# Kernel optimization log

Measured on AMD Instinct MI355X. Metric: run time of the kernel, lower is better.

Reference implementation:

```python
import jax, jax.numpy as jnp
import numpy as np

MODEL_DIM = 1024
HIDDEN = 2048
NUM_GROUPS = 2
EXPERTS_PER_GP = 4
NUM_EXPERTS = NUM_GROUPS * EXPERTS_PER_GP
TOP_K = 2
B, T = 2, 2048


def _swiglu(x):
    a, b = jnp.split(x, 2, axis=-1)
    return jax.nn.silu(a) * b


def setup_inputs() -> dict:
    key = jax.random.key(0)
    ks = jax.random.split(key, 7)
    s = 0.02  # init scale
    return {
        "x": jax.random.normal(ks[0], (B, T, MODEL_DIM), jnp.float32),
        # torch Linear weight layout [out_features, in_features]
        "w_in": jax.random.normal(ks[1], (HIDDEN * 2, MODEL_DIM), jnp.float32) * s,   # shared_in
        "w_out": jax.random.normal(ks[2], (MODEL_DIM, HIDDEN), jnp.float32) * s,      # shared_out
        "w1": jax.random.normal(ks[3], (HIDDEN * 2, MODEL_DIM), jnp.float32) * s,     # w1_shared
        "w2": jax.random.normal(ks[4], (NUM_EXPERTS, MODEL_DIM, HIDDEN), jnp.float32) * s,  # w2_expert stack
        "wg": jax.random.normal(ks[5], (NUM_GROUPS, MODEL_DIM), jnp.float32) * s,     # group_gate
        "we": jax.random.normal(ks[6], (NUM_EXPERTS, MODEL_DIM), jnp.float32) * s,    # expert_gate
        "gb": jnp.zeros((NUM_GROUPS,), jnp.float32),   # group_bias
        "eb": jnp.zeros((NUM_EXPERTS,), jnp.float32),  # expert_bias
    }


def reference(x, w_in, w_out, w1, w2, wg, we, gb, eb):
    Bs, Ts, C = x.shape
    S = Bs * Ts
    flat = x.reshape(S, C)

    # shared expert path
    shared = _swiglu(flat @ w_in.T) @ w_out.T                    # [S, C]

    # level-1: group gate (top-1)
    g_probs = jax.nn.softmax(flat @ wg.T + gb, axis=-1)          # [S, G]
    g_idx = jnp.argmax(g_probs, axis=-1)                         # [S]

    # level-2: expert gate masked to the chosen group
    e_logits = flat @ we.T + eb                                  # [S, E]
    egid = jnp.arange(NUM_EXPERTS) // EXPERTS_PER_GP             # expert -> group id
    masked = jnp.where(g_idx[:, None] == egid[None, :], e_logits, -jnp.inf)
    e_probs = jax.nn.softmax(masked, axis=-1)                    # zero outside group

    g_prob = jnp.take_along_axis(g_probs, g_idx[:, None], axis=1)  # [S, 1]
    p_expert = e_probs * g_prob                                  # [S, E]

    topv, topi = jax.lax.top_k(p_expert, TOP_K)                  # [S, k]

    # per-token per-expert combine weight (dense [S, E], rows k-sparse)
    w_se = jnp.zeros((S, NUM_EXPERTS), x.dtype).at[
        jnp.arange(S)[:, None], topi].add(topv)

    # w1 is shared across experts -> compute hidden once for all tokens
    h = _swiglu(flat @ w1.T)                                     # [S, H]

    # routed = sum_e w_se[:, e] * (h @ w2[e].T); scale commutes through linear
    routed = jnp.zeros_like(shared)
    for e in range(NUM_EXPERTS):  # small fixed expert count
        routed = routed + (h * w_se[:, e:e + 1]) @ w2[e].T

    return (shared + routed).reshape(Bs, Ts, C)
```

## Files before the change

kernel.cpp:

```cpp
#include <hip/hip_runtime.h>
#include <math.h>


#define C_DIM 1024
#define H_DIM 2048
#define S_TOK 4096

typedef _Float16 f16x8 __attribute__((ext_vector_type(8)));
typedef float f32x4 __attribute__((ext_vector_type(4)));

#define AS3(p) ((__attribute__((address_space(3))) void*)(p))
#define AS1c(p) ((const __attribute__((address_space(1))) void*)(p))

__global__ __launch_bounds__(256) void cvt_all(
    const float* __restrict__ x, const float* __restrict__ w_in,
    const float* __restrict__ w1, const float* __restrict__ w_out,
    const float* __restrict__ w2, _Float16* __restrict__ xh,
    _Float16* __restrict__ wprime, _Float16* __restrict__ wouth,
    _Float16* __restrict__ w2h) {
  int i = blockIdx.x * 256 + threadIdx.x;
  const float* s; _Float16* d; size_t soff, doff;
  if (i < 524288) { s = x; d = xh; soff = doff = (size_t)i; }
  else if (i < 1572864) {
    int n = i - 524288;
    int out_row = n >> 7, kc = n & 127;
    int wmat = out_row >> 12, r = out_row & 4095;
    int g = r >> 5, ii = r & 31;
    int src_row = (ii < 16) ? (g * 16 + ii) : (2048 + g * 16 + (ii - 16));
    s = wmat ? w1 : w_in; d = wprime;
    soff = (size_t)src_row * 128 + kc;
    doff = (size_t)n;
  } else if (i < 1835008) { int n = i - 1572864; s = w_out; d = wouth; soff = doff = (size_t)n; }
  else { int n = i - 1835008; s = w2; d = w2h; soff = doff = (size_t)n; }
  const float4* sp = reinterpret_cast<const float4*>(s) + soff * 2;
  float4 a = sp[0], b = sp[1];
  f16x8 h;
  h[0] = (_Float16)a.x; h[1] = (_Float16)a.y; h[2] = (_Float16)a.z; h[3] = (_Float16)a.w;
  h[4] = (_Float16)b.x; h[5] = (_Float16)b.y; h[6] = (_Float16)b.z; h[7] = (_Float16)b.w;
  reinterpret_cast<f16x8*>(d)[doff] = h;
}

__global__ __launch_bounds__(256) void gate_kernel(const float* __restrict__ x,
    const float* __restrict__ wg, const float* __restrict__ we,
    const float* __restrict__ gb, const float* __restrict__ eb,
    int* __restrict__ top2_e, float* __restrict__ top2_w) {
  const int lane = threadIdx.x & 63;
  const int token = blockIdx.x * 4 + (threadIdx.x >> 6);
  const float* xr = x + (size_t)token * C_DIM + lane * 16;
  float xv[16];
#pragma unroll
  for (int i = 0; i < 16; i += 4) {
    float4 t = *reinterpret_cast<const float4*>(xr + i);
    xv[i] = t.x; xv[i + 1] = t.y; xv[i + 2] = t.z; xv[i + 3] = t.w;
  }
  float dots[10];
#pragma unroll
  for (int g = 0; g < 10; ++g) {
    const float* wr = (g < 2 ? wg + (size_t)g * C_DIM : we + (size_t)(g - 2) * C_DIM) + lane * 16;
    float d = 0.f;
#pragma unroll
    for (int i = 0; i < 16; i += 4) {
      float4 t = *reinterpret_cast<const float4*>(wr + i);
      d += xv[i] * t.x + xv[i + 1] * t.y + xv[i + 2] * t.z + xv[i + 3] * t.w;
    }
#pragma unroll
    for (int off = 32; off > 0; off >>= 1) d += __shfl_xor(d, off);
    dots[g] = d;
  }
  if (lane != 0) return;
  float g0 = dots[0] + gb[0], g1 = dots[1] + gb[1];
  int gidx = (g0 >= g1) ? 0 : 1;
  float gm = fmaxf(g0, g1);
  float ex0 = expf(g0 - gm), ex1 = expf(g1 - gm);
  float gprob = (gidx == 0 ? ex0 : ex1) / (ex0 + ex1);
  const int base = gidx * 4;
  float el[4];
  float m = -1e30f;
#pragma unroll
  for (int jj = 0; jj < 4; ++jj) { el[jj] = dots[2 + base + jj] + eb[base + jj]; m = fmaxf(m, el[jj]); }
  float s = 0.f;
#pragma unroll
  for (int jj = 0; jj < 4; ++jj) { el[jj] = expf(el[jj] - m); s += el[jj]; }
  float p[8];
#pragma unroll
  for (int e = 0; e < 8; ++e) p[e] = 0.f;
#pragma unroll
  for (int jj = 0; jj < 4; ++jj) p[base + jj] = el[jj] / s * gprob;
  int i1 = 0; float v1 = -1.f;
#pragma unroll
  for (int e = 0; e < 8; ++e) if (p[e] > v1) { v1 = p[e]; i1 = e; }
  int i2 = -1; float v2 = -1.f;
#pragma unroll
  for (int e = 0; e < 8; ++e) if (e != i1 && p[e] > v2) { v2 = p[e]; i2 = e; }
  top2_e[token * 2] = i1;     top2_w[token * 2] = v1;
  top2_e[token * 2 + 1] = i2; top2_w[token * 2 + 1] = v2;
}

__global__ __launch_bounds__(256) void scanfill(const int* __restrict__ top2_e,
    const float* __restrict__ top2_w, int* __restrict__ offs_g,
    int* __restrict__ tok_list, float* __restrict__ scale_list,
    int* __restrict__ tok2slot) {
  __shared__ int cnt[8], offs[9], cur[8];
  const int tid = threadIdx.x;
  if (tid < 8) { cnt[tid] = 0; cur[tid] = 0; }
  __syncthreads();
  for (int i = tid; i < 2 * S_TOK; i += 256) atomicAdd(&cnt[top2_e[i]], 1);
  __syncthreads();
  if (tid == 0) {
    offs[0] = 0;
    for (int e = 0; e < 8; ++e) offs[e + 1] = offs[e] + cnt[e];
    for (int e = 0; e < 9; ++e) offs_g[e] = offs[e];
  }
  __syncthreads();
  for (int i = tid; i < 2 * S_TOK; i += 256) {
    int e = top2_e[i];
    int slot = atomicAdd(&cur[e], 1);
    int g = offs[e] + slot;
    tok_list[g] = i >> 1;
    scale_list[g] = top2_w[i];
    tok2slot[i] = g;
  }
}

__device__ __forceinline__ f16x8 frag_ld(const _Float16* t, int row, int u) {
  return *reinterpret_cast<const f16x8*>(t + row * 64 + ((u ^ (row & 7)) << 3));
}

#define BAR __builtin_amdgcn_s_barrier()
#define LGKM0 do { asm volatile("s_waitcnt lgkmcnt(0)" ::: "memory"); \
                   __builtin_amdgcn_sched_barrier(0); } while (0)
#define PRI1 __builtin_amdgcn_s_setprio(1)
#define PRI0 __builtin_amdgcn_s_setprio(0)

#define STAGEA(h_, t_) do { \
  const _Float16* s_ = aS[h_] + (size_t)(t_) * 64; \
  _Float16* d_ = lds + ((t_) & 1) * 32768 + (h_) * 8192 + grp0; \
  __builtin_amdgcn_global_load_lds(AS1c(s_), AS3(d_), 16, 0, 0); \
  __builtin_amdgcn_global_load_lds(AS1c(s_ + 65536), AS3(d_ + 4096), 16, 0, 0); \
} while (0)
#define STAGEB(h_, t_) do { \
  const _Float16* s_ = bS[h_] + (size_t)(t_) * 64; \
  _Float16* d_ = lds + ((t_) & 1) * 32768 + 16384 + (h_) * 8192 + grp0; \
  __builtin_amdgcn_global_load_lds(AS1c(s_), AS3(d_), 16, 0, 0); \
  __builtin_amdgcn_global_load_lds(AS1c(s_ + 65536), AS3(d_ + 4096), 16, 0, 0); \
} while (0)

#define LDA(MB_) do { _Pragma("unroll") for (int mm = 0; mm < 4; ++mm) \
  { _Pragma("unroll") for (int ks = 0; ks < 2; ++ks) \
    af[mm][ks] = frag_ld(At, wm * 128 + (MB_) + mm * 16 + lr, ks * 4 + lq); } } while (0)
#define LDB(DST_, CB_) do { _Pragma("unroll") for (int nn = 0; nn < 2; ++nn) \
  { _Pragma("unroll") for (int ks = 0; ks < 2; ++ks) \
    DST_[nn][ks] = frag_ld(Bt, wn * 64 + (CB_) + nn * 16 + lr, ks * 4 + lq); } } while (0)
#define QUAD(MB_, BF_, NB_) do { \
  _Pragma("unroll") for (int ks = 0; ks < 2; ++ks) \
  _Pragma("unroll") for (int mm = 0; mm < 4; ++mm) \
  _Pragma("unroll") for (int nn = 0; nn < 2; ++nn) \
    acc[(MB_) + mm][(NB_) + nn] = __builtin_amdgcn_mfma_f32_16x16x32_f16( \
        af[mm][ks], BF_[nn][ks], acc[(MB_) + mm][(NB_) + nn], 0, 0, 0); \
} while (0)

__global__ __launch_bounds__(512, 2) void gemm_fused_swiglu(
    const _Float16* __restrict__ A, const _Float16* __restrict__ Wp,
    _Float16* __restrict__ H1, _Float16* __restrict__ H2) {
  __shared__ _Float16 lds[65536];
  const int tid = threadIdx.x;
  const int lane = tid & 63;
  const int wid = tid >> 6;
  const int wm = wid >> 2, wn = wid & 3;
  const int lr = lane & 15, lq = lane >> 4;

  const int bid = blockIdx.x;
  const int xcd = bid & 7, j = bid >> 3;
  const int nb = xcd * 4 + (j & 3);
  const int mb = j >> 2;
  const int row0 = mb * 256;
  const int colg0 = nb * 256;

  const int rA = tid >> 3, uA = tid & 7;
  const int grp0 = (tid & ~63) << 3;
  const int swz = (uA ^ (rA & 7)) << 3;
  const _Float16* aS[2];
  const _Float16* bS[2];
#pragma unroll
  for (int h = 0; h < 2; ++h) {
    aS[h] = A  + (size_t)(row0  + h * 128 + rA) * 1024 + swz;
    bS[h] = Wp + (size_t)(colg0 + h * 128 + rA) * 1024 + swz;
  }

  STAGEB(0, 0); STAGEB(1, 0); STAGEA(0, 0); STAGEA(1, 0);
  STAGEB(0, 1); STAGEB(1, 1); STAGEA(0, 1); STAGEA(1, 1);
  asm volatile("s_waitcnt vmcnt(8)" ::: "memory");
  BAR;

  f32x4 acc[8][4] = {};
  f16x8 af[4][2], bf[2][2], bf2[2][2];

  for (int t = 0; t < 16; ++t) {
    const _Float16* At = lds + (t & 1) * 32768;
    const _Float16* Bt = At + 16384;
    LDA(0); LDB(bf, 0);
    BAR; LGKM0; PRI1; QUAD(0, bf, 0); PRI0; BAR;
    LDB(bf2, 32);
    BAR; LGKM0; PRI1; QUAD(0, bf2, 2); PRI0; BAR;
    LDA(64);
    if (t < 14) { STAGEB(0, t + 2); STAGEB(1, t + 2); }
    BAR; LGKM0; PRI1; QUAD(4, bf, 0); PRI0; BAR;
    if (t < 14) { STAGEA(0, t + 2); STAGEA(1, t + 2); }
    BAR; PRI1; QUAD(4, bf2, 2); PRI0;
    if (t <= 13) { asm volatile("s_waitcnt vmcnt(8)" ::: "memory"); }
    else if (t == 14) { asm volatile("s_waitcnt vmcnt(0)" ::: "memory"); }
    BAR;
  }

  _Float16* Hd = (colg0 >= 4096) ? H2 : H1;
  const int col0h = (colg0 & 4095) >> 1;
#pragma unroll
  for (int mm = 0; mm < 8; ++mm)
#pragma unroll
    for (int np = 0; np < 2; ++np)
#pragma unroll
      for (int r = 0; r < 4; ++r) {
        float a = acc[mm][np * 2][r];
        float b = acc[mm][np * 2 + 1][r];
        float h = (a / (1.0f + __expf(-a))) * b;
        int row = wm * 128 + mm * 16 + lq * 4 + r;
        int hcol = wn * 32 + np * 16 + lr;
        lds[row * 128 + ((((hcol >> 3) ^ (row & 7)) << 3) | (hcol & 7))] = (_Float16)h;
      }
  __syncthreads();
#pragma unroll
  for (int i = 0; i < 8; ++i) {
    int c = tid + i * 512;
    int row = c >> 4, bblk = c & 15;
    f16x8 v = *reinterpret_cast<const f16x8*>(lds + row * 128 + ((bblk ^ (row & 7)) << 3));
    *reinterpret_cast<f16x8*>(Hd + (size_t)(row0 + row) * H_DIM + col0h + bblk * 8) = v;
  }
}

#define OSTAGE(t_) do { int buf_ = ((t_) & 1) * 8192; \
  _Pragma("unroll") for (int i_ = 0; i_ < 2; ++i_) { \
    __builtin_amdgcn_global_load_lds(AS1c(aG[i_] + (size_t)(t_) * 64), AS3(aL[i_] + buf_), 16, 0, 0); \
    __builtin_amdgcn_global_load_lds(AS1c(bG[i_] + (size_t)(t_) * 64), AS3(bL[i_] + buf_), 16, 0, 0); } \
} while (0)

__global__ __launch_bounds__(512, 4) void gemm_out(
    const _Float16* __restrict__ H1, const _Float16* __restrict__ H2,
    const _Float16* __restrict__ Wout, const _Float16* __restrict__ W2,
    const int* __restrict__ offs_g, const int* __restrict__ tok_list,
    const float* __restrict__ scale_list,
    float* __restrict__ out, _Float16* __restrict__ routed) {
  __shared__ _Float16 AtF[2 * 128 * 64];
  __shared__ _Float16 BtF[2 * 128 * 64];
  __shared__ float sse[128];
  const int tid = threadIdx.x;
  const int lane = tid & 63;
  const int wid = tid >> 6;
  const int wm = wid >> 2, wn = wid & 3;
  const int lr = lane & 15, lq = lane >> 4;

  const int b = blockIdx.x;
  const bool shared_role = (b < 256);
  int rb, cb, offs_e = 0, n_e = 0;
  const _Float16* Bp;
  if (shared_role) {
    rb = b >> 3; cb = b & 7;
    Bp = Wout;
  } else {
    int eb2 = b - 256;
    int e = eb2 >> 8; rb = (eb2 >> 3) & 31; cb = eb2 & 7;
    offs_e = offs_g[e]; n_e = offs_g[e + 1] - offs_e;
    if (rb * 128 >= n_e) return;
    Bp = W2 + (size_t)e * C_DIM * H_DIM;
    if (tid < 128) {
      int lrr = rb * 128 + tid;
      sse[tid] = (lrr < n_e) ? scale_list[offs_e + lrr] : 0.f;
    }
  }

  const _Float16* aG[2];
  const _Float16* bG[2];
  _Float16* aL[2];
  _Float16* bL[2];
#pragma unroll
  for (int i = 0; i < 2; ++i) {
    int c = tid + i * 512;
    int row = c >> 3, u = c & 7;
    int swz = (u ^ (row & 7)) << 3;
    const _Float16* rowbase;
    if (shared_role) {
      rowbase = H1 + (size_t)(rb * 128 + row) * H_DIM;
    } else {
      int lrr = rb * 128 + row;
      int gs = offs_e + (lrr < n_e ? lrr : n_e - 1);
      rowbase = H2 + (size_t)tok_list[gs] * H_DIM;
    }
    aG[i] = rowbase + swz;
    bG[i] = Bp + (size_t)(cb * 128 + row) * H_DIM + swz;
    aL[i] = AtF + ((c & ~63) << 3);
    bL[i] = BtF + ((c & ~63) << 3);
  }

  OSTAGE(0); OSTAGE(1);
  asm volatile("s_waitcnt vmcnt(4)" ::: "memory");
  BAR;

  f32x4 acc[4][2] = {};
  for (int t = 0; t < 32; ++t) {
    const _Float16* Ab = AtF + (t & 1) * 8192;
    const _Float16* Bb = BtF + (t & 1) * 8192;
    f16x8 af[4][2], bfr[2][2];
#pragma unroll
    for (int m = 0; m < 4; ++m)
#pragma unroll
      for (int ks = 0; ks < 2; ++ks)
        af[m][ks] = frag_ld(Ab, wm * 64 + m * 16 + lr, ks * 4 + lq);
#pragma unroll
    for (int n = 0; n < 2; ++n)
#pragma unroll
      for (int ks = 0; ks < 2; ++ks)
        bfr[n][ks] = frag_ld(Bb, wn * 32 + n * 16 + lr, ks * 4 + lq);
    BAR; LGKM0;
    PRI1;
#pragma unroll
    for (int m = 0; m < 4; ++m)
#pragma unroll
      for (int n = 0; n < 2; ++n)
        acc[m][n] = __builtin_amdgcn_mfma_f32_16x16x32_f16(af[m][0], bfr[n][0], acc[m][n], 0, 0, 0);
    PRI0;
    BAR;
    if (t < 30) OSTAGE(t + 2);
    BAR;
    PRI1;
#pragma unroll
    for (int m = 0; m < 4; ++m)
#pragma unroll
      for (int n = 0; n < 2; ++n)
        acc[m][n] = __builtin_amdgcn_mfma_f32_16x16x32_f16(af[m][1], bfr[n][1], acc[m][n], 0, 0, 0);
    PRI0;
    if (t < 30) { asm volatile("s_waitcnt vmcnt(4)" ::: "memory"); }
    else if (t == 30) { asm volatile("s_waitcnt vmcnt(0)" ::: "memory"); }
    BAR;
  }

#pragma unroll
  for (int m = 0; m < 4; ++m)
#pragma unroll
    for (int n = 0; n < 2; ++n)
#pragma unroll
      for (int r = 0; r < 4; ++r) {
        int rloc = wm * 64 + m * 16 + (lq << 2) + r;
        int col = cb * 128 + wn * 32 + n * 16 + lr;
        if (shared_role) {
          out[(size_t)(rb * 128 + rloc) * C_DIM + col] = acc[m][n][r];
        } else {
          int lrr = rb * 128 + rloc;
          if (lrr < n_e)
            routed[(size_t)(offs_e + lrr) * C_DIM + col] =
                (_Float16)(sse[rloc] * acc[m][n][r]);
        }
      }
}

__global__ __launch_bounds__(256) void combine_final(float* __restrict__ out,
    const _Float16* __restrict__ routed, const int* __restrict__ tok2slot) {
  const int t = blockIdx.x * 2 + (threadIdx.x >> 7);
  const int cp = (threadIdx.x & 127) << 3;
  const int s0 = tok2slot[t * 2], s1 = tok2slot[t * 2 + 1];
  f16x8 r0 = *reinterpret_cast<const f16x8*>(routed + (size_t)s0 * C_DIM + cp);
  f16x8 r1 = *reinterpret_cast<const f16x8*>(routed + (size_t)s1 * C_DIM + cp);
  float* op = out + (size_t)t * C_DIM + cp;
  float4 o0 = *reinterpret_cast<const float4*>(op);
  float4 o1 = *reinterpret_cast<const float4*>(op + 4);
  o0.x += (float)r0[0] + (float)r1[0];
  o0.y += (float)r0[1] + (float)r1[1];
  o0.z += (float)r0[2] + (float)r1[2];
  o0.w += (float)r0[3] + (float)r1[3];
  o1.x += (float)r0[4] + (float)r1[4];
  o1.y += (float)r0[5] + (float)r1[5];
  o1.z += (float)r0[6] + (float)r1[6];
  o1.w += (float)r0[7] + (float)r1[7];
  *reinterpret_cast<float4*>(op) = o0;
  *reinterpret_cast<float4*>(op + 4) = o1;
}

extern "C" void kernel_launch(void* const* d_in, const int* in_sizes, int n_in,
                              void* d_out, int out_size, void* d_ws, size_t ws_size,
                              hipStream_t stream) {
  const float* x     = (const float*)d_in[0];
  const float* w_in  = (const float*)d_in[1];
  const float* w_out = (const float*)d_in[2];
  const float* w1    = (const float*)d_in[3];
  const float* w2    = (const float*)d_in[4];
  const float* wg    = (const float*)d_in[5];
  const float* we    = (const float*)d_in[6];
  const float* gb    = (const float*)d_in[7];
  const float* eb    = (const float*)d_in[8];
  float* out = (float*)d_out;

  char* ws = (char*)d_ws;
  const size_t MB = 1u << 20;
  _Float16* xh     = (_Float16*)(ws + 0 * MB);
  _Float16* wprime = (_Float16*)(ws + 8 * MB);
  _Float16* routed = (_Float16*)(ws + 0 * MB);
  _Float16* wouth  = (_Float16*)(ws + 24 * MB);
  _Float16* w2h    = (_Float16*)(ws + 28 * MB);
  _Float16* H1     = (_Float16*)(ws + 60 * MB);
  _Float16* H2     = (_Float16*)(ws + 76 * MB);
  char* sm = ws + 92 * MB;
  int*   offs_g     = (int*)(sm);
  int*   top2_e     = (int*)(sm + 64);
  float* top2_w     = (float*)(sm + 64 + 32768);
  int*   tok_list   = (int*)(sm + 64 + 65536);
  float* scale_list = (float*)(sm + 64 + 98304);
  int*   tok2slot   = (int*)(sm + 64 + 131072);

  cvt_all<<<15360, 256, 0, stream>>>(x, w_in, w1, w_out, w2,
                                     xh, wprime, wouth, w2h);
  gate_kernel<<<1024, 256, 0, stream>>>(x, wg, we, gb, eb, top2_e, top2_w);
  scanfill<<<1, 256, 0, stream>>>(top2_e, top2_w, offs_g, tok_list,
                                  scale_list, tok2slot);

  gemm_fused_swiglu<<<512, 512, 0, stream>>>(xh, wprime, H1, H2);

  gemm_out<<<2304, 512, 0, stream>>>(H1, H2, wouth, w2h, offs_g, tok_list,
                                     scale_list, out, routed);
  combine_final<<<2048, 256, 0, stream>>>(out, routed, tok2slot);
}
```

Before: 347.9 us.

## Use 256x256 tiles in output GEMM with expert segments padded to 256

The output GEMM moves from 128x128 tiles (2304 blocks, many idle) to 256x256 tiles with the same LDS-staged, interleaved MFMA schedule used by the first GEMM. Each expert's token segment is now padded to a multiple of 256 in scanfill, with padding slots filled with token 0 and scale 0, so routed blocks map onto a flat padded slot range and no row bounds checks are needed. The routed epilogue writes through a swizzled LDS tile to get vectorized stores. The change aims for more operand reuse and less wasted launch overhead, at the cost of extra compute on padding rows and fewer blocks (224) available for the machine.

```diff
diff --git a/kernel.cpp b/kernel.cpp
--- a/kernel.cpp
+++ b/kernel.cpp
@@ -97,7 +97,7 @@
 }
 
 __global__ __launch_bounds__(256) void scanfill(const int* __restrict__ top2_e,
-    const float* __restrict__ top2_w, int* __restrict__ offs_g,
+    const float* __restrict__ top2_w, int* __restrict__ offs_pad,
     int* __restrict__ tok_list, float* __restrict__ scale_list,
     int* __restrict__ tok2slot) {
   __shared__ int cnt[8], offs[9], cur[8];
@@ -108,9 +108,12 @@
   __syncthreads();
   if (tid == 0) {
     offs[0] = 0;
-    for (int e = 0; e < 8; ++e) offs[e + 1] = offs[e] + cnt[e];
-    for (int e = 0; e < 9; ++e) offs_g[e] = offs[e];
-  }
+    for (int e = 0; e < 8; ++e) offs[e + 1] = offs[e] + ((cnt[e] + 255) & ~255);
+    for (int e = 0; e < 9; ++e) offs_pad[e] = offs[e];
+  }
+  __syncthreads();
+  const int ptot = offs[8];
+  for (int i = tid; i < ptot; i += 256) { tok_list[i] = 0; scale_list[i] = 0.f; }
   __syncthreads();
   for (int i = tid; i < 2 * S_TOK; i += 256) {
     int e = top2_e[i];
@@ -131,19 +134,6 @@
                    __builtin_amdgcn_sched_barrier(0); } while (0)
 #define PRI1 __builtin_amdgcn_s_setprio(1)
 #define PRI0 __builtin_amdgcn_s_setprio(0)
-
-#define STAGEA(h_, t_) do { \
-  const _Float16* s_ = aS[h_] + (size_t)(t_) * 64; \
-  _Float16* d_ = lds + ((t_) & 1) * 32768 + (h_) * 8192 + grp0; \
-  __builtin_amdgcn_global_load_lds(AS1c(s_), AS3(d_), 16, 0, 0); \
-  __builtin_amdgcn_global_load_lds(AS1c(s_ + 65536), AS3(d_ + 4096), 16, 0, 0); \
-} while (0)
-#define STAGEB(h_, t_) do { \
-  const _Float16* s_ = bS[h_] + (size_t)(t_) * 64; \
-  _Float16* d_ = lds + ((t_) & 1) * 32768 + 16384 + (h_) * 8192 + grp0; \
-  __builtin_amdgcn_global_load_lds(AS1c(s_), AS3(d_), 16, 0, 0); \
-  __builtin_amdgcn_global_load_lds(AS1c(s_ + 65536), AS3(d_ + 4096), 16, 0, 0); \
-} while (0)
 
 #define LDA(MB_) do { _Pragma("unroll") for (int mm = 0; mm < 4; ++mm) \
   { _Pragma("unroll") for (int ks = 0; ks < 2; ++ks) \
@@ -157,6 +147,19 @@
   _Pragma("unroll") for (int nn = 0; nn < 2; ++nn) \
     acc[(MB_) + mm][(NB_) + nn] = __builtin_amdgcn_mfma_f32_16x16x32_f16( \
         af[mm][ks], BF_[nn][ks], acc[(MB_) + mm][(NB_) + nn], 0, 0, 0); \
+} while (0)
+
+#define STAGEA(h_, t_) do { \
+  const _Float16* s_ = aS[h_] + (size_t)(t_) * 64; \
+  _Float16* d_ = lds + ((t_) & 1) * 32768 + (h_) * 8192 + grp0; \
+  __builtin_amdgcn_global_load_lds(AS1c(s_), AS3(d_), 16, 0, 0); \
+  __builtin_amdgcn_global_load_lds(AS1c(s_ + 65536), AS3(d_ + 4096), 16, 0, 0); \
+} while (0)
+#define STAGEB(h_, t_) do { \
+  const _Float16* s_ = bS[h_] + (size_t)(t_) * 64; \
+  _Float16* d_ = lds + ((t_) & 1) * 32768 + 16384 + (h_) * 8192 + grp0; \
+  __builtin_amdgcn_global_load_lds(AS1c(s_), AS3(d_), 16, 0, 0); \
+  __builtin_amdgcn_global_load_lds(AS1c(s_ + 65536), AS3(d_ + 4096), 16, 0, 0); \
 } while (0)
 
 __global__ __launch_bounds__(512, 2) void gemm_fused_swiglu(
@@ -237,21 +240,21 @@
   }
 }
 
-#define OSTAGE(t_) do { int buf_ = ((t_) & 1) * 8192; \
-  _Pragma("unroll") for (int i_ = 0; i_ < 2; ++i_) { \
-    __builtin_amdgcn_global_load_lds(AS1c(aG[i_] + (size_t)(t_) * 64), AS3(aL[i_] + buf_), 16, 0, 0); \
-    __builtin_amdgcn_global_load_lds(AS1c(bG[i_] + (size_t)(t_) * 64), AS3(bL[i_] + buf_), 16, 0, 0); } \
-} while (0)
-
-__global__ __launch_bounds__(512, 4) void gemm_out(
+#define OSTGB(i_, t_) __builtin_amdgcn_global_load_lds( \
+    AS1c(bP[i_] + (size_t)(t_) * 64), \
+    AS3(lds + ((t_) & 1) * 32768 + 16384 + (i_) * 4096 + grp0), 16, 0, 0)
+#define OSTGA(i_, t_) __builtin_amdgcn_global_load_lds( \
+    AS1c(aP[i_] + (size_t)(t_) * 64), \
+    AS3(lds + ((t_) & 1) * 32768 + (i_) * 4096 + grp0), 16, 0, 0)
+
+__global__ __launch_bounds__(512, 2) void gemm_out256(
     const _Float16* __restrict__ H1, const _Float16* __restrict__ H2,
     const _Float16* __restrict__ Wout, const _Float16* __restrict__ W2,
-    const int* __restrict__ offs_g, const int* __restrict__ tok_list,
+    const int* __restrict__ offs_pad, const int* __restrict__ tok_list,
     const float* __restrict__ scale_list,
     float* __restrict__ out, _Float16* __restrict__ routed) {
-  __shared__ _Float16 AtF[2 * 128 * 64];
-  __shared__ _Float16 BtF[2 * 128 * 64];
-  __shared__ float sse[128];
+  __shared__ _Float16 lds[65536];
+  __shared__ float sse[256];
   const int tid = threadIdx.x;
   const int lane = tid & 63;
   const int wid = tid >> 6;
@@ -259,106 +262,103 @@
   const int lr = lane & 15, lq = lane >> 4;
 
   const int b = blockIdx.x;
-  const bool shared_role = (b < 256);
-  int rb, cb, offs_e = 0, n_e = 0;
+  const bool shared_role = (b < 64);
+  int sb, cb, p0 = 0;
   const _Float16* Bp;
   if (shared_role) {
-    rb = b >> 3; cb = b & 7;
+    sb = b >> 2; cb = b & 3;
     Bp = Wout;
   } else {
-    int eb2 = b - 256;
-    int e = eb2 >> 8; rb = (eb2 >> 3) & 31; cb = eb2 & 7;
-    offs_e = offs_g[e]; n_e = offs_g[e + 1] - offs_e;
-    if (rb * 128 >= n_e) return;
+    int idx = b - 64;
+    sb = idx >> 2; cb = idx & 3;
+    p0 = sb * 256;
+    if (p0 >= offs_pad[8]) return;
+    int e = 0;
+#pragma unroll
+    for (int k = 1; k < 8; ++k) e += (offs_pad[k] <= p0) ? 1 : 0;
     Bp = W2 + (size_t)e * C_DIM * H_DIM;
-    if (tid < 128) {
-      int lrr = rb * 128 + tid;
-      sse[tid] = (lrr < n_e) ? scale_list[offs_e + lrr] : 0.f;
+    if (tid < 256) sse[tid] = scale_list[p0 + tid];
+  }
+
+  const int rA = tid >> 3, uA = tid & 7;
+  const int grp0 = (tid & ~63) << 3;
+  const int swz = (uA ^ (rA & 7)) << 3;
+  const _Float16* aP[4];
+  const _Float16* bP[4];
+#pragma unroll
+  for (int h = 0; h < 2; ++h)
+#pragma unroll
+    for (int s = 0; s < 2; ++s) {
+      int arow = h * 128 + s * 64 + rA;
+      const _Float16* abase;
+      if (shared_role) abase = H1 + (size_t)(sb * 256 + arow) * H_DIM;
+      else             abase = H2 + (size_t)tok_list[p0 + arow] * H_DIM;
+      aP[h * 2 + s] = abase + swz;
+      bP[h * 2 + s] = Bp + (size_t)(cb * 256 + arow) * H_DIM + swz;
     }
-  }
-
-  const _Float16* aG[2];
-  const _Float16* bG[2];
-  _Float16* aL[2];
-  _Float16* bL[2];
-#pragma unroll
-  for (int i = 0; i < 2; ++i) {
-    int c = tid + i * 512;
-    int row = c >> 3, u = c & 7;
-    int swz = (u ^ (row & 7)) << 3;
-    const _Float16* rowbase;
-    if (shared_role) {
-      rowbase = H1 + (size_t)(rb * 128 + row) * H_DIM;
-    } else {
-      int lrr = rb * 128 + row;
-      int gs = offs_e + (lrr < n_e ? lrr : n_e - 1);
-      rowbase = H2 + (size_t)tok_list[gs] * H_DIM;
-    }
-    aG[i] = rowbase + swz;
-    bG[i] = Bp + (size_t)(cb * 128 + row) * H_DIM + swz;
-    aL[i] = AtF + ((c & ~63) << 3);
-    bL[i] = BtF + ((c & ~63) << 3);
-  }
-
-  OSTAGE(0); OSTAGE(1);
-  asm volatile("s_waitcnt vmcnt(4)" ::: "memory");
+
+  OSTGB(0, 0); OSTGB(1, 0); OSTGB(2, 0); OSTGB(3, 0);
+  OSTGA(0, 0); OSTGA(1, 0); OSTGA(2, 0); OSTGA(3, 0);
+  OSTGB(0, 1); OSTGB(1, 1); OSTGB(2, 1); OSTGB(3, 1);
+  OSTGA(0, 1); OSTGA(1, 1); OSTGA(2, 1); OSTGA(3, 1);
+  asm volatile("s_waitcnt vmcnt(8)" ::: "memory");
   BAR;
 
-  f32x4 acc[4][2] = {};
+  f32x4 acc[8][4] = {};
+  f16x8 af[4][2], bf[2][2], bf2[2][2];
+
   for (int t = 0; t < 32; ++t) {
-    const _Float16* Ab = AtF + (t & 1) * 8192;
-    const _Float16* Bb = BtF + (t & 1) * 8192;
-    f16x8 af[4][2], bfr[2][2];
-#pragma unroll
-    for (int m = 0; m < 4; ++m)
-#pragma unroll
-      for (int ks = 0; ks < 2; ++ks)
-        af[m][ks] = frag_ld(Ab, wm * 64 + m * 16 + lr, ks * 4 + lq);
-#pragma unroll
-    for (int n = 0; n < 2; ++n)
-#pragma unroll
-      for (int ks = 0; ks < 2; ++ks)
-        bfr[n][ks] = frag_ld(Bb, wn * 32 + n * 16 + lr, ks * 4 + lq);
-    BAR; LGKM0;
-    PRI1;
-#pragma unroll
-    for (int m = 0; m < 4; ++m)
-#pragma unroll
-      for (int n = 0; n < 2; ++n)
-        acc[m][n] = __builtin_amdgcn_mfma_f32_16x16x32_f16(af[m][0], bfr[n][0], acc[m][n], 0, 0, 0);
-    PRI0;
-    BAR;
-    if (t < 30) OSTAGE(t + 2);
-    BAR;
-    PRI1;
-#pragma unroll
-    for (int m = 0; m < 4; ++m)
-#pragma unroll
-      for (int n = 0; n < 2; ++n)
-        acc[m][n] = __builtin_amdgcn_mfma_f32_16x16x32_f16(af[m][1], bfr[n][1], acc[m][n], 0, 0, 0);
-    PRI0;
-    if (t < 30) { asm volatile("s_waitcnt vmcnt(4)" ::: "memory"); }
+    const _Float16* At = lds + (t & 1) * 32768;
+    const _Float16* Bt = At + 16384;
+    LDA(0); LDB(bf, 0);
+    BAR; LGKM0; PRI1; QUAD(0, bf, 0); PRI0; BAR;
+    LDB(bf2, 32);
+    BAR; LGKM0; PRI1; QUAD(0, bf2, 2); PRI0; BAR;
+    LDA(64);
+    if (t < 30) { OSTGB(0, t + 2); OSTGB(1, t + 2); OSTGB(2, t + 2); OSTGB(3, t + 2); }
+    BAR; LGKM0; PRI1; QUAD(4, bf, 0); PRI0; BAR;
+    if (t < 30) { OSTGA(0, t + 2); OSTGA(1, t + 2); OSTGA(2, t + 2); OSTGA(3, t + 2); }
+    BAR; PRI1; QUAD(4, bf2, 2); PRI0;
+    if (t <= 29) { asm volatile("s_waitcnt vmcnt(8)" ::: "memory"); }
     else if (t == 30) { asm volatile("s_waitcnt vmcnt(0)" ::: "memory"); }
     BAR;
   }
 
-#pragma unroll
-  for (int m = 0; m < 4; ++m)
-#pragma unroll
-    for (int n = 0; n < 2; ++n)
-#pragma unroll
-      for (int r = 0; r < 4; ++r) {
-        int rloc = wm * 64 + m * 16 + (lq << 2) + r;
-        int col = cb * 128 + wn * 32 + n * 16 + lr;
-        if (shared_role) {
-          out[(size_t)(rb * 128 + rloc) * C_DIM + col] = acc[m][n][r];
-        } else {
-          int lrr = rb * 128 + rloc;
-          if (lrr < n_e)
-            routed[(size_t)(offs_e + lrr) * C_DIM + col] =
-                (_Float16)(sse[rloc] * acc[m][n][r]);
+  if (shared_role) {
+#pragma unroll
+    for (int mm = 0; mm < 8; ++mm)
+#pragma unroll
+      for (int nn = 0; nn < 4; ++nn)
+#pragma unroll
+        for (int r = 0; r < 4; ++r) {
+          int rloc = wm * 128 + mm * 16 + lq * 4 + r;
+          int col = cb * 256 + wn * 64 + nn * 16 + lr;
+          out[(size_t)(sb * 256 + rloc) * C_DIM + col] = acc[mm][nn][r];
         }
-      }
+  } else {
+#pragma unroll
+    for (int mm = 0; mm < 8; ++mm)
+#pragma unroll
+      for (int nn = 0; nn < 4; ++nn)
+#pragma unroll
+        for (int r = 0; r < 4; ++r) {
+          int rloc = wm * 128 + mm * 16 + lq * 4 + r;
+          int col = wn * 64 + nn * 16 + lr;
+          float v = sse[rloc] * acc[mm][nn][r];
+          int u = col >> 3;
+          int us = (u & 24) | ((u ^ rloc) & 7);
+          lds[rloc * 256 + (us << 3) + (col & 7)] = (_Float16)v;
+        }
+    __syncthreads();
+#pragma unroll
+    for (int i = 0; i < 16; ++i) {
+      int c = tid + i * 512;
+      int row = c >> 5, u = c & 31;
+      int us = (u & 24) | ((u ^ row) & 7);
+      f16x8 v = *reinterpret_cast<const f16x8*>(lds + row * 256 + (us << 3));
+      *reinterpret_cast<f16x8*>(routed + (size_t)(p0 + row) * C_DIM + cb * 256 + u * 8) = v;
+    }
+  }
 }
 
 __global__ __launch_bounds__(256) void combine_final(float* __restrict__ out,
@@ -407,22 +407,22 @@
   _Float16* H1     = (_Float16*)(ws + 60 * MB);
   _Float16* H2     = (_Float16*)(ws + 76 * MB);
   char* sm = ws + 92 * MB;
-  int*   offs_g     = (int*)(sm);
-  int*   top2_e     = (int*)(sm + 64);
-  float* top2_w     = (float*)(sm + 64 + 32768);
-  int*   tok_list   = (int*)(sm + 64 + 65536);
-  float* scale_list = (float*)(sm + 64 + 98304);
-  int*   tok2slot   = (int*)(sm + 64 + 131072);
+  int*   offs_pad   = (int*)(sm);
+  int*   top2_e     = (int*)(sm + 1024);
+  float* top2_w     = (float*)(sm + 1024 + 32768);
+  int*   tok_list   = (int*)(sm + 1024 + 65536);
+  float* scale_list = (float*)(sm + 1024 + 106496);
+  int*   tok2slot   = (int*)(sm + 1024 + 147456);
 
   cvt_all<<<15360, 256, 0, stream>>>(x, w_in, w1, w_out, w2,
                                      xh, wprime, wouth, w2h);
   gate_kernel<<<1024, 256, 0, stream>>>(x, wg, we, gb, eb, top2_e, top2_w);
-  scanfill<<<1, 256, 0, stream>>>(top2_e, top2_w, offs_g, tok_list,
+  scanfill<<<1, 256, 0, stream>>>(top2_e, top2_w, offs_pad, tok_list,
                                   scale_list, tok2slot);
 
   gemm_fused_swiglu<<<512, 512, 0, stream>>>(xh, wprime, H1, H2);
 
-  gemm_out<<<2304, 512, 0, stream>>>(H1, H2, wouth, w2h, offs_g, tok_list,
-                                     scale_list, out, routed);
+  gemm_out256<<<224, 512, 0, stream>>>(H1, H2, wouth, w2h, offs_pad, tok_list,
+                                       scale_list, out, routed);
   combine_final<<<2048, 256, 0, stream>>>(out, routed, tok2slot);
 }
```

Result: faster. 339.2 us (-2.5%).
